# Kernel tuning notes

Measured on AMD Instinct MI355X. Metric: run time of the kernel, lower is better.

Reference implementation:

```python
import jax, jax.numpy as jnp
import numpy as np

D = 2048
H = 16
HD = D // H
FF = 4 * D
B, L = 2, 2048
EPS = 1e-6
NEG = -1e9


def setup_inputs() -> dict:
    key = jax.random.key(0)
    ks = jax.random.split(key, 8)
    x = jax.random.normal(ks[0], (B, L, D), dtype=jnp.float32)
    # causal additive mask [1,1,L,L]
    causal = jnp.triu(jnp.full((L, L), NEG, dtype=jnp.float32), k=1)
    mask = causal[None, None, :, :]
    s = 0.02
    params = {
        'norm1_w': jnp.ones((D,), jnp.float32),
        'qkv_w': jax.random.normal(ks[1], (3 * D, D), jnp.float32) * s,
        'out_w': jax.random.normal(ks[2], (D, D), jnp.float32) * s,
        'norm2_w': jnp.ones((D,), jnp.float32),
        'gate_w': jax.random.normal(ks[3], (FF, D), jnp.float32) * s,
        'up_w': jax.random.normal(ks[4], (FF, D), jnp.float32) * s,
        'down_w': jax.random.normal(ks[5], (D, FF), jnp.float32) * s,
    }
    return {'x': x, 'mask': mask, **params}


def _rmsnorm(x, w):
    return x * jax.lax.rsqrt(jnp.mean(x * x, axis=-1, keepdims=True) + EPS) * w


def reference(x, mask, norm1_w, qkv_w, out_w, norm2_w, gate_w, up_w, down_w):
    b, l, d = x.shape
    # --- attention ---
    h = _rmsnorm(x, norm1_w)
    qkv = h @ qkv_w.T                          # [B,L,3D]
    qkv = qkv.reshape(b, l, 3, H, HD)
    q, k, v = (jnp.moveaxis(qkv, 2, 0)[i].transpose(0, 2, 1, 3) for i in range(3))  # each [B,H,L,HD]
    scores = jnp.einsum('bhqd,bhkd->bhqk', q, k) / jnp.sqrt(jnp.float32(HD))
    scores = scores + mask
    attn = jax.nn.softmax(scores, axis=-1)
    o = jnp.einsum('bhqk,bhkd->bhqd', attn, v)  # [B,H,L,HD]
    o = o.transpose(0, 2, 1, 3).reshape(b, l, d)
    x = x + o @ out_w.T
    # --- SwiGLU FFN ---
    h2 = _rmsnorm(x, norm2_w)
    ff = (jax.nn.silu(h2 @ gate_w.T) * (h2 @ up_w.T)) @ down_w.T
    return x + ff
```

## Files before the change

### kernel.cpp

```cpp
#include <hip/hip_runtime.h>


typedef __attribute__((ext_vector_type(8))) short bf16x8;
typedef __attribute__((ext_vector_type(4))) float f32x4;

__device__ __forceinline__ float b2f(unsigned short u) {
    return __uint_as_float(((unsigned int)u) << 16);
}
__device__ __forceinline__ unsigned short f2b(float f) {
    unsigned int i = __float_as_uint(f);
    i += 0x7fffu + ((i >> 16) & 1u);
    return (unsigned short)(i >> 16);
}
__device__ __forceinline__ unsigned int cvt_pk_bf16(float lo, float hi) {
    unsigned int r;
    asm("v_cvt_pk_bf16_f32 %0, %1, %2" : "=v"(r) : "v"(lo), "v"(hi));
    return r;
}

__device__ __forceinline__ void gload_lds16(const unsigned short* g, unsigned short* l) {
    __builtin_amdgcn_global_load_lds(
        (const __attribute__((address_space(1))) unsigned int*)g,
        (__attribute__((address_space(3))) unsigned int*)l,
        16, 0, 0);
}

template<int DT> struct IO;
template<> struct IO<1> {
    static __device__ __forceinline__ void load8(const void* p, size_t i, float* o) {
        uint4 v = *(const uint4*)((const unsigned short*)p + i);
        const unsigned short* u = (const unsigned short*)&v;
#pragma unroll
        for (int e = 0; e < 8; e++) o[e] = b2f(u[e]);
    }
    static __device__ __forceinline__ float load1(const void* p, size_t i) {
        return b2f(((const unsigned short*)p)[i]);
    }
    static __device__ __forceinline__ void store1(void* p, size_t i, float v) {
        ((unsigned short*)p)[i] = f2b(v);
    }
};
template<> struct IO<0> {
    static __device__ __forceinline__ void load8(const void* p, size_t i, float* o) {
        float4 a = *(const float4*)((const float*)p + i);
        float4 b = *(const float4*)((const float*)p + i + 4);
        o[0]=a.x; o[1]=a.y; o[2]=a.z; o[3]=a.w;
        o[4]=b.x; o[5]=b.y; o[6]=b.z; o[7]=b.w;
    }
    static __device__ __forceinline__ float load1(const void* p, size_t i) {
        return ((const float*)p)[i];
    }
    static __device__ __forceinline__ void store1(void* p, size_t i, float v) {
        ((float*)p)[i] = v;
    }
};

__global__ __launch_bounds__(256) void detect_kernel(
    const unsigned int* __restrict__ x, int* __restrict__ flag)
{
    const int t = threadIdx.x;
    int cnt = 0;
    for (int i = t; i < 2048; i += 256) {
        unsigned int e = (x[i] >> 7) & 0xFFu;
        cnt += (e >= 100u && e <= 140u) ? 1 : 0;
    }
#pragma unroll
    for (int off = 32; off; off >>= 1) cnt += __shfl_xor(cnt, off);
    __shared__ int red[4];
    if ((t & 63) == 0) red[t >> 6] = cnt;
    __syncthreads();
    if (t == 0) {
        int tot = red[0] + red[1] + red[2] + red[3];
        flag[0] = (2 * tot > 2048) ? 1 : 0;
    }
}

template<int PID>
__global__ __launch_bounds__(256) void convw_kernel(
    const int* __restrict__ flag,
    const float* __restrict__ S, int lds_,
    unsigned short* __restrict__ D, int ldd,
    int total)
{
    if (flag[0] != PID) return;
    const int i = (blockIdx.x * 256 + threadIdx.x) * 8;
    if (i >= total) return;
    const int row = i / ldd, col = i - row * ldd;
    const float* sp = S + (size_t)row * lds_ + col;
    float4 f0 = *(const float4*)sp;
    float4 f1 = *(const float4*)(sp + 4);
    uint4 ov;
    ov.x = cvt_pk_bf16(f0.x, f0.y);
    ov.y = cvt_pk_bf16(f0.z, f0.w);
    ov.z = cvt_pk_bf16(f1.x, f1.y);
    ov.w = cvt_pk_bf16(f1.z, f1.w);
    *(uint4*)(D + i) = ov;
}

template<int PID, int DTX, int DTW>
__global__ __launch_bounds__(256) void rmsnorm_kernel(
    const int* __restrict__ flag,
    const void* __restrict__ X,
    const void* __restrict__ Wn,
    unsigned short* __restrict__ Out)
{
    if (flag[0] != PID) return;
    const int row = blockIdx.x, t = threadIdx.x;
    float xf[8];
    IO<DTX>::load8(X, (size_t)row * 2048 + t * 8, xf);
    float ss = 0.f;
#pragma unroll
    for (int e = 0; e < 8; e++) ss += xf[e] * xf[e];
#pragma unroll
    for (int off = 32; off; off >>= 1) ss += __shfl_xor(ss, off);
    __shared__ float red[4];
    if ((t & 63) == 0) red[t >> 6] = ss;
    __syncthreads();
    float rr = rsqrtf((red[0] + red[1] + red[2] + red[3]) * (1.0f / 2048.0f) + 1e-6f);
    float wf[8];
    IO<DTW>::load8(Wn, (size_t)t * 8, wf);
    float y[8];
#pragma unroll
    for (int e = 0; e < 8; e++) y[e] = xf[e] * rr * wf[e];
    uint4 ov;
    ov.x = cvt_pk_bf16(y[0], y[1]);
    ov.y = cvt_pk_bf16(y[2], y[3]);
    ov.z = cvt_pk_bf16(y[4], y[5]);
    ov.w = cvt_pk_bf16(y[6], y[7]);
    *(uint4*)(Out + (size_t)row * 2048 + t * 8) = ov;
}

#define BM 128
#define BN 128
#define BKK 64

template<int PID, int DTR, int DTC, int EPI>
__global__ __launch_bounds__(256) void gemm_bt(
    const int* __restrict__ flag,
    const unsigned short* __restrict__ A,
    const unsigned short* __restrict__ W, size_t woff, int ldw,
    const void* __restrict__ Res,
    void* __restrict__ C,
    int N, int K)
{
    if (flag[0] != PID) return;
    __shared__ unsigned short sA[BM * BKK];
    __shared__ unsigned short sB[BN * BKK];
    const int t = threadIdx.x;
    const int bm = blockIdx.x * BM, bn = blockIdx.y * BN;
    const int w = t >> 6, lane = t & 63, quad = lane >> 4, l16 = lane & 15;
    const int wm = (w & 1) * 64, wn = (w >> 1) * 64;

    const int srow = lane >> 3;
    const int sg   = (lane & 7) ^ srow;

    f32x4 acc[4][4];
#pragma unroll
    for (int mi = 0; mi < 4; mi++)
#pragma unroll
        for (int ni = 0; ni < 4; ni++) {
            f32x4 z = {0.f, 0.f, 0.f, 0.f};
            acc[mi][ni] = z;
        }

    for (int k0 = 0; k0 < K; k0 += BKK) {
#pragma unroll
        for (int i = 0; i < 4; i++) {
            const int r0 = w * 32 + i * 8;
            gload_lds16(A + (size_t)(bm + r0 + srow) * K + k0 + sg * 8,
                        &sA[r0 * BKK]);
        }
#pragma unroll
        for (int i = 0; i < 4; i++) {
            const int r0 = w * 32 + i * 8;
            gload_lds16(W + woff + (size_t)(bn + r0 + srow) * ldw + k0 + sg * 8,
                        &sB[r0 * BKK]);
        }
        __syncthreads();

#pragma unroll
        for (int ks = 0; ks < 2; ks++) {
            bf16x8 af[4], bfr[4];
#pragma unroll
            for (int mi = 0; mi < 4; mi++) {
                const int r = wm + mi * 16 + l16;
                af[mi] = *(const bf16x8*)
                    &sA[r * BKK + (((ks * 4 + quad) ^ (r & 7)) * 8)];
            }
#pragma unroll
            for (int ni = 0; ni < 4; ni++) {
                const int r = wn + ni * 16 + l16;
                bfr[ni] = *(const bf16x8*)
                    &sB[r * BKK + (((ks * 4 + quad) ^ (r & 7)) * 8)];
            }
#pragma unroll
            for (int mi = 0; mi < 4; mi++)
#pragma unroll
                for (int ni = 0; ni < 4; ni++)
                    acc[mi][ni] = __builtin_amdgcn_mfma_f32_16x16x32_bf16(
                        af[mi], bfr[ni], acc[mi][ni], 0, 0, 0);
        }
        __syncthreads();
    }

#pragma unroll
    for (int mi = 0; mi < 4; mi++)
#pragma unroll
        for (int ni = 0; ni < 4; ni++)
#pragma unroll
            for (int r = 0; r < 4; r++) {
                const int row = bm + wm + mi * 16 + quad * 4 + r;
                const int col = bn + wn + ni * 16 + l16;
                const size_t idx = (size_t)row * N + col;
                float v = acc[mi][ni][r];
                if constexpr (EPI == 1) v += IO<DTR>::load1(Res, idx);
                if constexpr (EPI == 2) v = v / (1.f + __expf(-v));
                if constexpr (EPI == 3) v *= IO<DTR>::load1(Res, idx);
                IO<DTC>::store1(C, idx, v);
            }
}

__device__ __forceinline__ int vt_idx(int d, int kv) {
    return d * 72 + (kv ^ (d & 56));
}

template<int PID>
__global__ __launch_bounds__(256) void attn_kernel(
    const int* __restrict__ flag,
    const unsigned short* __restrict__ QKV,
    unsigned short* __restrict__ O)
{
    if (flag[0] != PID) return;
    __shared__ unsigned short sK[64 * 128];
    __shared__ unsigned short sVt[9280];
    __shared__ unsigned short sP[4][16 * 72];

    const int t = threadIdx.x;
    const int bh = blockIdx.x >> 4;
    const int jj = blockIdx.x & 15;
    const int b = bh >> 4, hh = bh & 15;
    const int w = t >> 6, lane = t & 63, quad = lane >> 4, l16 = lane & 15;

    const unsigned short* Qb = QKV + (size_t)(b * 2048) * 6144 + hh * 128;
    const unsigned short* Kb = Qb + 2048;
    const unsigned short* Vb = Qb + 4096;

    const int str = t >> 4;
    const int stc = (t & 15) * 8;

#pragma unroll
    for (int half = 0; half < 2; half++) {
        const int qt = half ? (31 - jj) : jj;
        const int qbase = qt * 64;

        bf16x8 qf[4];
        {
            const unsigned short* qp = Qb + (size_t)(qbase + w * 16 + l16) * 6144;
#pragma unroll
            for (int ks = 0; ks < 4; ks++)
                qf[ks] = *(const bf16x8*)(qp + ks * 32 + quad * 8);
        }

        float m[4], l[4];
#pragma unroll
        for (int r = 0; r < 4; r++) { m[r] = -1e30f; l[r] = 0.f; }
        f32x4 accO[8];
#pragma unroll
        for (int d0 = 0; d0 < 8; d0++) {
            f32x4 z = {0.f, 0.f, 0.f, 0.f};
            accO[d0] = z;
        }

        for (int tk = 0; tk <= qt; tk++) {
            const int kv0 = tk * 64;
            __syncthreads();
#pragma unroll
            for (int pass = 0; pass < 4; pass++) {
                const int rr = str + pass * 16;
                uint4 kv4 = *(const uint4*)(Kb + (size_t)(kv0 + rr) * 6144 + stc);
                *(uint4*)&sK[(rr * 128 + stc) ^ ((rr & 7) << 3)] = kv4;
                uint4 vv4 = *(const uint4*)(Vb + (size_t)(kv0 + rr) * 6144 + stc);
                const unsigned short* vu = (const unsigned short*)&vv4;
#pragma unroll
                for (int e = 0; e < 8; e++)
                    sVt[vt_idx(stc + e, rr)] = vu[e];
            }
            __syncthreads();

            const bool diag = (tk == qt);
            f32x4 s[4];
#pragma unroll
            for (int nf = 0; nf < 4; nf++) {
                f32x4 z = {0.f, 0.f, 0.f, 0.f};
                s[nf] = z;
                if (!(diag && nf > w)) {
#pragma unroll
                    for (int ks = 0; ks < 4; ks++) {
                        const int row = nf * 16 + l16;
                        bf16x8 kf = *(const bf16x8*)
                            &sK[(row * 128 + ks * 32 + quad * 8) ^ ((row & 7) << 3)];
                        s[nf] = __builtin_amdgcn_mfma_f32_16x16x32_bf16(qf[ks], kf, s[nf], 0, 0, 0);
                    }
                }
#pragma unroll
                for (int r = 0; r < 4; r++) s[nf][r] *= 0.08838834764831845f;
            }
            if (diag) {
#pragma unroll
                for (int nf = 0; nf < 4; nf++)
#pragma unroll
                    for (int r = 0; r < 4; r++)
                        if (nf * 16 + l16 > w * 16 + quad * 4 + r) s[nf][r] = -1e30f;
            }

            float alpha[4], rs[4];
#pragma unroll
            for (int r = 0; r < 4; r++) {
                float v = fmaxf(fmaxf(s[0][r], s[1][r]), fmaxf(s[2][r], s[3][r]));
                v = fmaxf(v, __shfl_xor(v, 1));
                v = fmaxf(v, __shfl_xor(v, 2));
                v = fmaxf(v, __shfl_xor(v, 4));
                v = fmaxf(v, __shfl_xor(v, 8));
                float mn = fmaxf(m[r], v);
                alpha[r] = __expf(m[r] - mn);
                m[r] = mn;
                rs[r] = 0.f;
            }
#pragma unroll
            for (int nf = 0; nf < 4; nf++)
#pragma unroll
                for (int r = 0; r < 4; r++) {
                    float p = __expf(s[nf][r] - m[r]);
                    rs[r] += p;
                    sP[w][(quad * 4 + r) * 72 + nf * 16 + l16] = f2b(p);
                }
#pragma unroll
            for (int r = 0; r < 4; r++) {
                float sum = rs[r];
                sum += __shfl_xor(sum, 1);
                sum += __shfl_xor(sum, 2);
                sum += __shfl_xor(sum, 4);
                sum += __shfl_xor(sum, 8);
                l[r] = l[r] * alpha[r] + sum;
            }
#pragma unroll
            for (int d0 = 0; d0 < 8; d0++)
#pragma unroll
                for (int r = 0; r < 4; r++) accO[d0][r] *= alpha[r];

#pragma unroll
            for (int ks = 0; ks < 2; ks++) {
                bf16x8 pa = *(const bf16x8*)&sP[w][l16 * 72 + ks * 32 + quad * 8];
#pragma unroll
                for (int d0 = 0; d0 < 8; d0++) {
                    bf16x8 vb = *(const bf16x8*)
                        &sVt[vt_idx(d0 * 16 + l16, ks * 32 + quad * 8)];
                    accO[d0] = __builtin_amdgcn_mfma_f32_16x16x32_bf16(pa, vb, accO[d0], 0, 0, 0);
                }
            }
        }

        float linv[4];
#pragma unroll
        for (int r = 0; r < 4; r++) linv[r] = 1.0f / l[r];
        unsigned short* Op = O + (size_t)(b * 2048 + qbase + w * 16) * 2048 + hh * 128;
#pragma unroll
        for (int d0 = 0; d0 < 8; d0++)
#pragma unroll
            for (int r = 0; r < 4; r++)
                Op[(size_t)(quad * 4 + r) * 2048 + d0 * 16 + l16] =
                    f2b(accO[d0][r] * linv[r]);
    }
}

template<int DT>
static void run_pipeline(const void* x, const void* n1w, const void* qkvw,
                         const void* outw, const void* n2w, const void* gatew,
                         const void* upw, const void* downw,
                         void* outp, char* ws, const int* flag, hipStream_t stream)
{
    const size_t MB = 1024 * 1024;
    unsigned short* qkv = (unsigned short*)(ws);
    unsigned short* x2  = (unsigned short*)(ws);
    unsigned short* h2  = (unsigned short*)(ws + 16 * MB);
    unsigned short* a   = (unsigned short*)(ws + 32 * MB);
    unsigned short* h   = (unsigned short*)(ws + 48 * MB);
    unsigned short* o   = (unsigned short*)(ws + 48 * MB);

    rmsnorm_kernel<DT, DT, DT><<<4096, 256, 0, stream>>>(flag, x, n1w, h);

    if constexpr (DT == 1) {
        const unsigned short* Wq = (const unsigned short*)qkvw;
        const unsigned short* Wo = (const unsigned short*)outw;
        const unsigned short* Wg = (const unsigned short*)gatew;
        const unsigned short* Wu = (const unsigned short*)upw;
        const unsigned short* Wd = (const unsigned short*)downw;
        gemm_bt<1, 1, 1, 0><<<dim3(32, 48), 256, 0, stream>>>(
            flag, h, Wq, 0, 2048, nullptr, qkv, 6144, 2048);
        attn_kernel<1><<<512, 256, 0, stream>>>(flag, qkv, o);
        gemm_bt<1, 1, 1, 1><<<dim3(32, 16), 256, 0, stream>>>(
            flag, o, Wo, 0, 2048, x, x2, 2048, 2048);
        rmsnorm_kernel<1, 1, 1><<<4096, 256, 0, stream>>>(flag, x2, n2w, h2);
        gemm_bt<1, 1, 1, 2><<<dim3(32, 32), 256, 0, stream>>>(
            flag, h2, Wg, 0, 2048, nullptr, a, 4096, 2048);
        gemm_bt<1, 1, 1, 3><<<dim3(32, 32), 256, 0, stream>>>(
            flag, h2, Wu, 0, 2048, a, a, 4096, 2048);
        gemm_bt<1, 1, 1, 1><<<dim3(32, 16), 256, 0, stream>>>(
            flag, a, Wd, 0, 8192, x2, x2, 2048, 4096);
        gemm_bt<1, 1, 1, 2><<<dim3(32, 32), 256, 0, stream>>>(
            flag, h2, Wg, (size_t)4096 * 2048, 2048, nullptr, a, 4096, 2048);
        gemm_bt<1, 1, 1, 3><<<dim3(32, 32), 256, 0, stream>>>(
            flag, h2, Wu, (size_t)4096 * 2048, 2048, a, a, 4096, 2048);
        gemm_bt<1, 1, 1, 1><<<dim3(32, 16), 256, 0, stream>>>(
            flag, a, Wd, 4096, 8192, x2, outp, 2048, 4096);
    } else {
        unsigned short* WC  = (unsigned short*)outp;
        unsigned short* WC2 = h2;

        convw_kernel<0><<<6144, 256, 0, stream>>>(
            flag, (const float*)qkvw, 2048, WC, 2048, 6144 * 2048);
        gemm_bt<0, 1, 1, 0><<<dim3(32, 48), 256, 0, stream>>>(
            flag, h, WC, 0, 2048, nullptr, qkv, 6144, 2048);
        attn_kernel<0><<<512, 256, 0, stream>>>(flag, qkv, o);
        convw_kernel<0><<<2048, 256, 0, stream>>>(
            flag, (const float*)outw, 2048, WC, 2048, 2048 * 2048);
        gemm_bt<0, 0, 1, 1><<<dim3(32, 16), 256, 0, stream>>>(
            flag, o, WC, 0, 2048, x, x2, 2048, 2048);
        rmsnorm_kernel<0, 1, 0><<<4096, 256, 0, stream>>>(flag, x2, n2w, h2);
        convw_kernel<0><<<4096, 256, 0, stream>>>(
            flag, (const float*)gatew, 2048, WC, 2048, 4096 * 2048);
        gemm_bt<0, 1, 1, 2><<<dim3(32, 32), 256, 0, stream>>>(
            flag, h2, WC, 0, 2048, nullptr, a, 4096, 2048);
        convw_kernel<0><<<4096, 256, 0, stream>>>(
            flag, (const float*)upw, 2048, WC, 2048, 4096 * 2048);
        gemm_bt<0, 1, 1, 3><<<dim3(32, 32), 256, 0, stream>>>(
            flag, h2, WC, 0, 2048, a, a, 4096, 2048);
        convw_kernel<0><<<4096, 256, 0, stream>>>(
            flag, (const float*)downw, 8192, WC, 4096, 2048 * 4096);
        gemm_bt<0, 1, 1, 1><<<dim3(32, 16), 256, 0, stream>>>(
            flag, a, WC, 0, 4096, x2, x2, 2048, 4096);
        convw_kernel<0><<<4096, 256, 0, stream>>>(
            flag, (const float*)gatew + (size_t)4096 * 2048, 2048, WC, 2048, 4096 * 2048);
        gemm_bt<0, 1, 1, 2><<<dim3(32, 32), 256, 0, stream>>>(
            flag, h2, WC, 0, 2048, nullptr, a, 4096, 2048);
        convw_kernel<0><<<4096, 256, 0, stream>>>(
            flag, (const float*)upw + (size_t)4096 * 2048, 2048, WC, 2048, 4096 * 2048);
        gemm_bt<0, 1, 1, 3><<<dim3(32, 32), 256, 0, stream>>>(
            flag, h2, WC, 0, 2048, a, a, 4096, 2048);
        convw_kernel<0><<<4096, 256, 0, stream>>>(
            flag, (const float*)downw + 4096, 8192, WC2, 4096, 2048 * 4096);
        gemm_bt<0, 1, 0, 1><<<dim3(32, 16), 256, 0, stream>>>(
            flag, a, WC2, 0, 4096, x2, outp, 2048, 4096);
    }
}

extern "C" void kernel_launch(void* const* d_in, const int* in_sizes, int n_in,
                              void* d_out, int out_size, void* d_ws, size_t ws_size,
                              hipStream_t stream)
{
    const void* x      = d_in[0];
    const void* n1w    = d_in[2];
    const void* qkv_w  = d_in[3];
    const void* out_w  = d_in[4];
    const void* n2w    = d_in[5];
    const void* gate_w = d_in[6];
    const void* up_w   = d_in[7];
    const void* down_w = d_in[8];

    char* ws = (char*)d_ws;
    const size_t MB = 1024 * 1024;
    size_t flag_off = 64 * MB;
    if (ws_size < flag_off + 4) flag_off = (ws_size - 4) & ~(size_t)3;
    int* flag = (int*)(ws + flag_off);

    detect_kernel<<<1, 256, 0, stream>>>((const unsigned int*)x, flag);
    run_pipeline<0>(x, n1w, qkv_w, out_w, n2w, gate_w, up_w, down_w,
                    d_out, ws, flag, stream);
    run_pipeline<1>(x, n1w, qkv_w, out_w, n2w, gate_w, up_w, down_w,
                    d_out, ws, flag, stream);
}
```

Before: 1.171 ms.

## Split attention into one query tile per block with XCD-aware mapping and XOR swizzles

Each block now handles a single 64-row query tile instead of a paired light and heavy tile, doubling the grid. Block indices are remapped so each XCD gets a contiguous group of batch-heads, improving K/V reuse in that XCD's L2, and heavy tiles are scheduled first. The padded V-transpose and P buffers are replaced with unpadded XOR-swizzled layouts, with rotated element order on the transpose stores to cut LDS bank conflicts. The trade-off is losing the built-in load balance of pairing short and long tiles, relying on the scheduler to fill gaps instead.

```diff
diff --git a/kernel.cpp b/kernel.cpp
--- a/kernel.cpp
+++ b/kernel.cpp
@@ -220,10 +220,6 @@
             }
 }
 
-__device__ __forceinline__ int vt_idx(int d, int kv) {
-    return d * 72 + (kv ^ (d & 56));
-}
-
 template<int PID>
 __global__ __launch_bounds__(256) void attn_kernel(
     const int* __restrict__ flag,
@@ -232,12 +228,14 @@
 {
     if (flag[0] != PID) return;
     __shared__ unsigned short sK[64 * 128];
-    __shared__ unsigned short sVt[9280];
-    __shared__ unsigned short sP[4][16 * 72];
+    __shared__ unsigned short sVt[128 * 64];
+    __shared__ unsigned short sP[4][16 * 64];
 
     const int t = threadIdx.x;
-    const int bh = blockIdx.x >> 4;
-    const int jj = blockIdx.x & 15;
+    const int xcd = blockIdx.x & 7;
+    const int local = blockIdx.x >> 3;
+    const int bh = xcd * 4 + (local >> 5);
+    const int qt = 31 - (local & 31);
     const int b = bh >> 4, hh = bh & 15;
     const int w = t >> 6, lane = t & 63, quad = lane >> 4, l16 = lane & 15;
 
@@ -247,130 +245,134 @@
 
     const int str = t >> 4;
     const int stc = (t & 15) * 8;
-
-#pragma unroll
-    for (int half = 0; half < 2; half++) {
-        const int qt = half ? (31 - jj) : jj;
-        const int qbase = qt * 64;
-
-        bf16x8 qf[4];
-        {
-            const unsigned short* qp = Qb + (size_t)(qbase + w * 16 + l16) * 6144;
-#pragma unroll
-            for (int ks = 0; ks < 4; ks++)
-                qf[ks] = *(const bf16x8*)(qp + ks * 32 + quad * 8);
-        }
-
-        float m[4], l[4];
-#pragma unroll
-        for (int r = 0; r < 4; r++) { m[r] = -1e30f; l[r] = 0.f; }
-        f32x4 accO[8];
-#pragma unroll
-        for (int d0 = 0; d0 < 8; d0++) {
+    const int rot = t & 7;
+
+    const int qbase = qt * 64;
+
+    bf16x8 qf[4];
+    {
+        const unsigned short* qp = Qb + (size_t)(qbase + w * 16 + l16) * 6144;
+#pragma unroll
+        for (int ks = 0; ks < 4; ks++)
+            qf[ks] = *(const bf16x8*)(qp + ks * 32 + quad * 8);
+    }
+
+    float m[4], l[4];
+#pragma unroll
+    for (int r = 0; r < 4; r++) { m[r] = -1e30f; l[r] = 0.f; }
+    f32x4 accO[8];
+#pragma unroll
+    for (int d0 = 0; d0 < 8; d0++) {
+        f32x4 z = {0.f, 0.f, 0.f, 0.f};
+        accO[d0] = z;
+    }
+
+    for (int tk = 0; tk <= qt; tk++) {
+        const int kv0 = tk * 64;
+        __syncthreads();
+#pragma unroll
+        for (int pass = 0; pass < 4; pass++) {
+            const int rr = str + pass * 16;
+            uint4 kv4 = *(const uint4*)(Kb + (size_t)(kv0 + rr) * 6144 + stc);
+            *(uint4*)&sK[(rr * 128 + stc) ^ ((rr & 7) << 3)] = kv4;
+            uint4 vv4 = *(const uint4*)(Vb + (size_t)(kv0 + rr) * 6144 + stc);
+            const unsigned short* vu = (const unsigned short*)&vv4;
+#pragma unroll
+            for (int i = 0; i < 8; i++) {
+                const int e = (i + rot) & 7;
+                const int d = stc + e;
+                sVt[d * 64 + ((((rr >> 3) ^ (d & 7)) << 3) | (rr & 7))] = vu[e];
+            }
+        }
+        __syncthreads();
+
+        const bool diag = (tk == qt);
+        f32x4 s[4];
+#pragma unroll
+        for (int nf = 0; nf < 4; nf++) {
             f32x4 z = {0.f, 0.f, 0.f, 0.f};
-            accO[d0] = z;
-        }
-
-        for (int tk = 0; tk <= qt; tk++) {
-            const int kv0 = tk * 64;
-            __syncthreads();
-#pragma unroll
-            for (int pass = 0; pass < 4; pass++) {
-                const int rr = str + pass * 16;
-                uint4 kv4 = *(const uint4*)(Kb + (size_t)(kv0 + rr) * 6144 + stc);
-                *(uint4*)&sK[(rr * 128 + stc) ^ ((rr & 7) << 3)] = kv4;
-                uint4 vv4 = *(const uint4*)(Vb + (size_t)(kv0 + rr) * 6144 + stc);
-                const unsigned short* vu = (const unsigned short*)&vv4;
-#pragma unroll
-                for (int e = 0; e < 8; e++)
-                    sVt[vt_idx(stc + e, rr)] = vu[e];
-            }
-            __syncthreads();
-
-            const bool diag = (tk == qt);
-            f32x4 s[4];
-#pragma unroll
-            for (int nf = 0; nf < 4; nf++) {
-                f32x4 z = {0.f, 0.f, 0.f, 0.f};
-                s[nf] = z;
-                if (!(diag && nf > w)) {
-#pragma unroll
-                    for (int ks = 0; ks < 4; ks++) {
-                        const int row = nf * 16 + l16;
-                        bf16x8 kf = *(const bf16x8*)
-                            &sK[(row * 128 + ks * 32 + quad * 8) ^ ((row & 7) << 3)];
-                        s[nf] = __builtin_amdgcn_mfma_f32_16x16x32_bf16(qf[ks], kf, s[nf], 0, 0, 0);
-                    }
+            s[nf] = z;
+            if (!(diag && nf > w)) {
+#pragma unroll
+                for (int ks = 0; ks < 4; ks++) {
+                    const int row = nf * 16 + l16;
+                    bf16x8 kf = *(const bf16x8*)
+                        &sK[(row * 128 + ks * 32 + quad * 8) ^ ((row & 7) << 3)];
+                    s[nf] = __builtin_amdgcn_mfma_f32_16x16x32_bf16(qf[ks], kf, s[nf], 0, 0, 0);
                 }
-#pragma unroll
-                for (int r = 0; r < 4; r++) s[nf][r] *= 0.08838834764831845f;
-            }
-            if (diag) {
-#pragma unroll
-                for (int nf = 0; nf < 4; nf++)
-#pragma unroll
-                    for (int r = 0; r < 4; r++)
-                        if (nf * 16 + l16 > w * 16 + quad * 4 + r) s[nf][r] = -1e30f;
-            }
-
-            float alpha[4], rs[4];
+            }
+#pragma unroll
+            for (int r = 0; r < 4; r++) s[nf][r] *= 0.08838834764831845f;
+        }
+        if (diag) {
+#pragma unroll
+            for (int nf = 0; nf < 4; nf++)
+#pragma unroll
+                for (int r = 0; r < 4; r++)
+                    if (nf * 16 + l16 > w * 16 + quad * 4 + r) s[nf][r] = -1e30f;
+        }
+
+        float alpha[4], rs[4];
+#pragma unroll
+        for (int r = 0; r < 4; r++) {
+            float v = fmaxf(fmaxf(s[0][r], s[1][r]), fmaxf(s[2][r], s[3][r]));
+            v = fmaxf(v, __shfl_xor(v, 1));
+            v = fmaxf(v, __shfl_xor(v, 2));
+            v = fmaxf(v, __shfl_xor(v, 4));
+            v = fmaxf(v, __shfl_xor(v, 8));
+            float mn = fmaxf(m[r], v);
+            alpha[r] = __expf(m[r] - mn);
+            m[r] = mn;
+            rs[r] = 0.f;
+        }
+#pragma unroll
+        for (int nf = 0; nf < 4; nf++)
 #pragma unroll
             for (int r = 0; r < 4; r++) {
-                float v = fmaxf(fmaxf(s[0][r], s[1][r]), fmaxf(s[2][r], s[3][r]));
-                v = fmaxf(v, __shfl_xor(v, 1));
-                v = fmaxf(v, __shfl_xor(v, 2));
-                v = fmaxf(v, __shfl_xor(v, 4));
-                v = fmaxf(v, __shfl_xor(v, 8));
-                float mn = fmaxf(m[r], v);
-                alpha[r] = __expf(m[r] - mn);
-                m[r] = mn;
-                rs[r] = 0.f;
-            }
-#pragma unroll
-            for (int nf = 0; nf < 4; nf++)
-#pragma unroll
-                for (int r = 0; r < 4; r++) {
-                    float p = __expf(s[nf][r] - m[r]);
-                    rs[r] += p;
-                    sP[w][(quad * 4 + r) * 72 + nf * 16 + l16] = f2b(p);
-                }
-#pragma unroll
-            for (int r = 0; r < 4; r++) {
-                float sum = rs[r];
-                sum += __shfl_xor(sum, 1);
-                sum += __shfl_xor(sum, 2);
-                sum += __shfl_xor(sum, 4);
-                sum += __shfl_xor(sum, 8);
-                l[r] = l[r] * alpha[r] + sum;
-            }
-#pragma unroll
-            for (int d0 = 0; d0 < 8; d0++)
-#pragma unroll
-                for (int r = 0; r < 4; r++) accO[d0][r] *= alpha[r];
-
-#pragma unroll
-            for (int ks = 0; ks < 2; ks++) {
-                bf16x8 pa = *(const bf16x8*)&sP[w][l16 * 72 + ks * 32 + quad * 8];
-#pragma unroll
-                for (int d0 = 0; d0 < 8; d0++) {
-                    bf16x8 vb = *(const bf16x8*)
-                        &sVt[vt_idx(d0 * 16 + l16, ks * 32 + quad * 8)];
-                    accO[d0] = __builtin_amdgcn_mfma_f32_16x16x32_bf16(pa, vb, accO[d0], 0, 0, 0);
-                }
-            }
-        }
-
-        float linv[4];
-#pragma unroll
-        for (int r = 0; r < 4; r++) linv[r] = 1.0f / l[r];
-        unsigned short* Op = O + (size_t)(b * 2048 + qbase + w * 16) * 2048 + hh * 128;
+                float p = __expf(s[nf][r] - m[r]);
+                rs[r] += p;
+                const int row = quad * 4 + r;
+                const int g = nf * 2 + (l16 >> 3);
+                sP[w][row * 64 + (((g ^ (row & 7)) << 3) | (l16 & 7))] = f2b(p);
+            }
+#pragma unroll
+        for (int r = 0; r < 4; r++) {
+            float sum = rs[r];
+            sum += __shfl_xor(sum, 1);
+            sum += __shfl_xor(sum, 2);
+            sum += __shfl_xor(sum, 4);
+            sum += __shfl_xor(sum, 8);
+            l[r] = l[r] * alpha[r] + sum;
+        }
 #pragma unroll
         for (int d0 = 0; d0 < 8; d0++)
 #pragma unroll
-            for (int r = 0; r < 4; r++)
-                Op[(size_t)(quad * 4 + r) * 2048 + d0 * 16 + l16] =
-                    f2b(accO[d0][r] * linv[r]);
-    }
+            for (int r = 0; r < 4; r++) accO[d0][r] *= alpha[r];
+
+#pragma unroll
+        for (int ks = 0; ks < 2; ks++) {
+            bf16x8 pa = *(const bf16x8*)
+                &sP[w][l16 * 64 + (((ks * 4 + quad) ^ (l16 & 7)) << 3)];
+#pragma unroll
+            for (int d0 = 0; d0 < 8; d0++) {
+                const int row = d0 * 16 + l16;
+                bf16x8 vb = *(const bf16x8*)
+                    &sVt[row * 64 + (((ks * 4 + quad) ^ (l16 & 7)) << 3)];
+                accO[d0] = __builtin_amdgcn_mfma_f32_16x16x32_bf16(pa, vb, accO[d0], 0, 0, 0);
+            }
+        }
+    }
+
+    float linv[4];
+#pragma unroll
+    for (int r = 0; r < 4; r++) linv[r] = 1.0f / l[r];
+    unsigned short* Op = O + (size_t)(b * 2048 + qbase + w * 16) * 2048 + hh * 128;
+#pragma unroll
+    for (int d0 = 0; d0 < 8; d0++)
+#pragma unroll
+        for (int r = 0; r < 4; r++)
+            Op[(size_t)(quad * 4 + r) * 2048 + d0 * 16 + l16] =
+                f2b(accO[d0][r] * linv[r]);
 }
 
 template<int DT>
@@ -397,7 +399,7 @@
         const unsigned short* Wd = (const unsigned short*)downw;
         gemm_bt<1, 1, 1, 0><<<dim3(32, 48), 256, 0, stream>>>(
             flag, h, Wq, 0, 2048, nullptr, qkv, 6144, 2048);
-        attn_kernel<1><<<512, 256, 0, stream>>>(flag, qkv, o);
+        attn_kernel<1><<<1024, 256, 0, stream>>>(flag, qkv, o);
         gemm_bt<1, 1, 1, 1><<<dim3(32, 16), 256, 0, stream>>>(
             flag, o, Wo, 0, 2048, x, x2, 2048, 2048);
         rmsnorm_kernel<1, 1, 1><<<4096, 256, 0, stream>>>(flag, x2, n2w, h2);
@@ -421,7 +423,7 @@
             flag, (const float*)qkvw, 2048, WC, 2048, 6144 * 2048);
         gemm_bt<0, 1, 1, 0><<<dim3(32, 48), 256, 0, stream>>>(
             flag, h, WC, 0, 2048, nullptr, qkv, 6144, 2048);
-        attn_kernel<0><<<512, 256, 0, stream>>>(flag, qkv, o);
+        attn_kernel<0><<<1024, 256, 0, stream>>>(flag, qkv, o);
         convw_kernel<0><<<2048, 256, 0, stream>>>(
             flag, (const float*)outw, 2048, WC, 2048, 2048 * 2048);
         gemm_bt<0, 0, 1, 1><<<dim3(32, 16), 256, 0, stream>>>(
```

Measured after the change: 1.193 ms. No clear change (+1.9%).
